# Performance work log

Measured on AMD Instinct MI355X. Metric: run time of the kernel, lower is better.

Reference implementation:

```python
import jax, jax.numpy as jnp
import numpy as np

EMB = 4096
NUM_EXPERTS = 64
TOP_K = 2
TOKENS = 16384


def setup_inputs() -> dict:
    key = jax.random.key(0)
    kx, kw, kb = jax.random.split(key, 3)
    x = jax.random.normal(kx, (TOKENS, EMB), dtype=jnp.float32)
    # nn.Linear(emb_size, num_experts): weight [num_experts, emb], bias [num_experts]
    W = jax.random.normal(kw, (NUM_EXPERTS, EMB), dtype=jnp.float32) / np.sqrt(EMB)
    b = jax.random.normal(kb, (NUM_EXPERTS,), dtype=jnp.float32) * 0.01
    return {"x": x, "W": W, "b": b}


def reference(x, W, b):
    # logits = x @ W.T + b  -> [tokens, num_experts]
    logits = jnp.einsum("td,ed->te", x, W) + b
    topk_val, topk_idx = jax.lax.top_k(logits, TOP_K)  # [tokens, k]
    probs = jax.nn.softmax(topk_val, axis=-1)
    return (topk_idx, probs)
```

## Files before the change

kernel.cpp:

```cpp
#include <hip/hip_runtime.h>

#define TOKENS 16384
#define EMB 4096
#define NEXP 64
#define BK 64

typedef __attribute__((ext_vector_type(8))) short short8;
typedef __attribute__((ext_vector_type(4))) float f32x4;
typedef __attribute__((ext_vector_type(4))) unsigned short ush4;

#define WP_USHORTS (3 * NEXP * EMB)
#define WP_FLOATS  (WP_USHORTS / 2)

__device__ __forceinline__ void gl_lds16(const void* g, void* lds) {
    __builtin_amdgcn_global_load_lds(
        (const __attribute__((address_space(1))) void*)g,
        (__attribute__((address_space(3))) void*)lds, 16, 0, 0);
}

__device__ __forceinline__ void split3(float x, unsigned short& h,
                                       unsigned short& m, unsigned short& l) {
    unsigned u = __float_as_uint(x);
    unsigned r = u + 0x7FFFu + ((u >> 16) & 1u);
    float hF = __uint_as_float(r & 0xFFFF0000u);
    h = (unsigned short)(r >> 16);
    float r1 = x - hF;
    unsigned u1 = __float_as_uint(r1);
    float mF = __uint_as_float(u1 & 0xFFFF0000u);
    m = (unsigned short)(u1 >> 16);
    float r2 = r1 - mF;
    l = (unsigned short)(__float_as_uint(r2) >> 16);
}

__global__ __launch_bounds__(256) void split_w(const float* __restrict__ W,
                                               unsigned short* __restrict__ Wp) {
    const int i = (blockIdx.x * 256 + threadIdx.x) * 4;
    const float4 v = *reinterpret_cast<const float4*>(W + i);
    ush4 h, m, l;
#pragma unroll
    for (int e = 0; e < 4; ++e) {
        unsigned short he, me, le;
        split3(reinterpret_cast<const float*>(&v)[e], he, me, le);
        h[e] = he; m[e] = me; l[e] = le;
    }
    *reinterpret_cast<ush4*>(Wp + i) = h;
    *reinterpret_cast<ush4*>(Wp + NEXP * EMB + i) = m;
    *reinterpret_cast<ush4*>(Wp + 2 * NEXP * EMB + i) = l;
}

template<int S>
__global__ __launch_bounds__(512, 4) void router_mfma(
    const float* __restrict__ x, const unsigned short* __restrict__ Wp,
    float* __restrict__ part)
{
    constexpr int KPER = EMB / S;
    constexpr int NCH  = KPER / BK;

    __shared__ unsigned short sB[3][192][BK];

    const int t  = threadIdx.x;
    const int w  = t >> 6;
    const int l  = t & 63;
    const int lr = l & 15;
    const int lo = l >> 4;
    const int tok0 = blockIdx.x * 128 + w * 16;
    const int kb   = blockIdx.y * KPER;

    const float* ax = x + (size_t)(tok0 + lr) * EMB + kb + lo * 8;

    const unsigned short* gb[3];
#pragma unroll
    for (int p = 0; p < 3; ++p)
        gb[p] = Wp + (size_t)(24 * w + 8 * p + (l >> 3)) * EMB + kb
              + 8 * ((l & 7) ^ ((l >> 3) & 7));

    f32x4 accH[4], accL[4];
#pragma unroll
    for (int et = 0; et < 4; ++et) {
        accH[et] = (f32x4){0.f, 0.f, 0.f, 0.f};
        accL[et] = (f32x4){0.f, 0.f, 0.f, 0.f};
    }

    float4 ac[2][2], an[2][2];
#pragma unroll
    for (int p = 0; p < 3; ++p)
        gl_lds16(gb[p], &sB[0][24 * w + 8 * p][0]);
#pragma unroll
    for (int h = 0; h < 2; ++h) {
        ac[h][0] = *reinterpret_cast<const float4*>(ax + 32 * h);
        ac[h][1] = *reinterpret_cast<const float4*>(ax + 32 * h + 4);
    }
#pragma unroll
    for (int p = 0; p < 3; ++p)
        gl_lds16(gb[p] + BK, &sB[1][24 * w + 8 * p][0]);

    int buf = 0;
#pragma unroll 1
    for (int ks = 0; ks < NCH; ++ks) {
        asm volatile("s_waitcnt vmcnt(3)" ::: "memory");
        __builtin_amdgcn_s_barrier();

        if (ks + 1 < NCH) {
#pragma unroll
            for (int h = 0; h < 2; ++h) {
                an[h][0] = *reinterpret_cast<const float4*>(ax + (ks + 1) * BK + 32 * h);
                an[h][1] = *reinterpret_cast<const float4*>(ax + (ks + 1) * BK + 32 * h + 4);
            }
        }
        if (ks + 2 < NCH) {
            const int sb = (buf == 0) ? 2 : buf - 1;
#pragma unroll
            for (int p = 0; p < 3; ++p)
                gl_lds16(gb[p] + (ks + 2) * BK, &sB[sb][24 * w + 8 * p][0]);
        }
        __builtin_amdgcn_sched_barrier(0);

#pragma unroll
        for (int h = 0; h < 2; ++h) {
            short8 aH, aM, aL;
#pragma unroll
            for (int e = 0; e < 4; ++e) {
                unsigned short he, me, le;
                split3(reinterpret_cast<const float*>(&ac[h][0])[e], he, me, le);
                aH[e] = (short)he; aM[e] = (short)me; aL[e] = (short)le;
                split3(reinterpret_cast<const float*>(&ac[h][1])[e], he, me, le);
                aH[4 + e] = (short)he; aM[4 + e] = (short)me; aL[4 + e] = (short)le;
            }
#pragma unroll
            for (int et = 0; et < 4; ++et) {
                const int sw = (((4 * h + lo) ^ (lr & 7)) * 8);
                const unsigned short* bp = &sB[buf][et * 16 + lr][sw];
                const short8 bH = *reinterpret_cast<const short8*>(bp);
                const short8 bM = *reinterpret_cast<const short8*>(bp + 64 * BK);
                const short8 bL = *reinterpret_cast<const short8*>(bp + 128 * BK);
                accH[et] = __builtin_amdgcn_mfma_f32_16x16x32_bf16(aH, bH, accH[et], 0, 0, 0);
                accL[et] = __builtin_amdgcn_mfma_f32_16x16x32_bf16(aH, bM, accL[et], 0, 0, 0);
                accL[et] = __builtin_amdgcn_mfma_f32_16x16x32_bf16(aM, bH, accL[et], 0, 0, 0);
                accL[et] = __builtin_amdgcn_mfma_f32_16x16x32_bf16(aM, bM, accL[et], 0, 0, 0);
                accL[et] = __builtin_amdgcn_mfma_f32_16x16x32_bf16(aH, bL, accL[et], 0, 0, 0);
                accL[et] = __builtin_amdgcn_mfma_f32_16x16x32_bf16(aL, bH, accL[et], 0, 0, 0);
            }
        }
#pragma unroll
        for (int h = 0; h < 2; ++h) { ac[h][0] = an[h][0]; ac[h][1] = an[h][1]; }
        buf = (buf == 2) ? 0 : buf + 1;
    }

    __syncthreads();
    float* sled = reinterpret_cast<float*>(&sB[0][0][0]) + w * 1024;
#pragma unroll
    for (int et = 0; et < 4; ++et)
#pragma unroll
        for (int j = 0; j < 4; ++j)
            sled[(et * 16 + lr) * 16 + lo * 4 + j] = accH[et][j] + accL[et][j];
#pragma unroll
    for (int r = 0; r < 16; ++r) {
        const int e = 4 * r + lo;
        part[(size_t)(blockIdx.y * NEXP + e) * TOKENS + tok0 + lr]
            = sled[e * 16 + lr];
    }
}

template<int S>
__global__ __launch_bounds__(256) void reduce_topk(
    const float* __restrict__ part, const float* __restrict__ b,
    float* __restrict__ out)
{
    __shared__ double sv[64][4][2];
    __shared__ int    si[64][4][2];
    const int t    = threadIdx.x;
    const int p4   = t & 3;
    const int slot = t >> 2;
    const int tok  = blockIdx.x * 64 + slot;

    double v[16];
#pragma unroll
    for (int j = 0; j < 16; ++j) v[j] = 0.0;
    for (int s = 0; s < S; ++s)
#pragma unroll
        for (int j = 0; j < 16; ++j)
            v[j] += (double)part[(size_t)((s << 6) + (p4 << 4) + j) * TOKENS + tok];
#pragma unroll
    for (int j = 0; j < 16; ++j) v[j] += (double)b[(p4 << 4) + j];

    double v1 = -1e300, v2 = -1e300; int i1 = 0, i2 = 0;
#pragma unroll
    for (int j = 0; j < 16; ++j) {
        const int e = (p4 << 4) + j;
        if (v[j] > v1)      { v2 = v1; i2 = i1; v1 = v[j]; i1 = e; }
        else if (v[j] > v2) { v2 = v[j]; i2 = e; }
    }
    sv[slot][p4][0] = v1; sv[slot][p4][1] = v2;
    si[slot][p4][0] = i1; si[slot][p4][1] = i2;
    __syncthreads();

    if (p4 == 0) {
        double m1 = -1e300, m2 = -1e300; int j1 = 0, j2 = 0;
#pragma unroll
        for (int p = 0; p < 4; ++p)
#pragma unroll
            for (int r = 0; r < 2; ++r) {
                const double vv = sv[slot][p][r]; const int ii = si[slot][p][r];
                if (vv > m1)      { m2 = m1; j2 = j1; m1 = vv; j1 = ii; }
                else if (vv > m2) { m2 = vv; j2 = ii; }
            }
        const float e2  = expf((float)(m2 - m1));
        const float inv = 1.0f / (1.0f + e2);
        out[2 * tok]     = (float)j1;
        out[2 * tok + 1] = (float)j2;
        out[2 * TOKENS + 2 * tok]     = inv;
        out[2 * TOKENS + 2 * tok + 1] = e2 * inv;
    }
}

extern "C" void kernel_launch(void* const* d_in, const int* in_sizes, int n_in,
                              void* d_out, int out_size, void* d_ws, size_t ws_size,
                              hipStream_t stream) {
    const float* x = (const float*)d_in[0];
    const float* W = (const float*)d_in[1];
    const float* b = (const float*)d_in[2];
    float* out = (float*)d_out;
    unsigned short* Wp = (unsigned short*)d_ws;
    float* part = (float*)d_ws + WP_FLOATS;

    split_w<<<dim3(NEXP * EMB / 1024), dim3(256), 0, stream>>>(W, Wp);

    const size_t base = (size_t)WP_FLOATS * 4;
    const size_t per  = (size_t)NEXP * TOKENS * 4;
    if (ws_size >= base + 4 * per) {
        router_mfma<4><<<dim3(TOKENS / 128, 4), dim3(512), 0, stream>>>(x, Wp, part);
        reduce_topk<4><<<dim3(TOKENS / 64), dim3(256), 0, stream>>>(part, b, out);
    } else if (ws_size >= base + 2 * per) {
        router_mfma<2><<<dim3(TOKENS / 128, 2), dim3(512), 0, stream>>>(x, Wp, part);
        reduce_topk<2><<<dim3(TOKENS / 64), dim3(256), 0, stream>>>(part, b, out);
    } else {
        router_mfma<1><<<dim3(TOKENS / 128, 1), dim3(512), 0, stream>>>(x, Wp, part);
        reduce_topk<1><<<dim3(TOKENS / 64), dim3(256), 0, stream>>>(part, b, out);
    }
}
```

Measured before the change: 81.00 us.

## Compute two token tiles per wave to reuse B fragments from LDS

The router GEMM block drops from 8 to 4 waves, and each wave now handles 32 tokens (two 16-row tiles). Each B fragment read from LDS therefore feeds twice as many MFMAs, which halves LDS read traffic per MFMA. The bf16 three-way split is rewritten to pack pairs with v_perm, cutting the ALU work that builds the A fragments. In exchange each thread holds more registers (double the accumulators and A staging), occupancy drops, and the epilogue uses a padded 33-stride LDS transpose.

Result: no change. 81.12 us (+0.2%).

```diff
diff --git a/kernel.cpp b/kernel.cpp
--- a/kernel.cpp
+++ b/kernel.cpp
@@ -32,6 +32,31 @@
     l = (unsigned short)(__float_as_uint(r2) >> 16);
 }
 
+__device__ __forceinline__ void split3_pair(float x0, float x1,
+        unsigned& hw, unsigned& mw, unsigned& lw) {
+    unsigned u0 = __float_as_uint(x0), u1 = __float_as_uint(x1);
+    unsigned r0 = u0 + 0x7FFFu + ((u0 >> 16) & 1u);
+    unsigned r1 = u1 + 0x7FFFu + ((u1 >> 16) & 1u);
+    hw = __builtin_amdgcn_perm(r1, r0, 0x07060302u);
+    float s0 = x0 - __uint_as_float(r0 & 0xFFFF0000u);
+    float s1 = x1 - __uint_as_float(r1 & 0xFFFF0000u);
+    unsigned v0 = __float_as_uint(s0), v1 = __float_as_uint(s1);
+    mw = __builtin_amdgcn_perm(v1, v0, 0x07060302u);
+    float t0 = s0 - __uint_as_float(v0 & 0xFFFF0000u);
+    float t1 = s1 - __uint_as_float(v1 & 0xFFFF0000u);
+    lw = __builtin_amdgcn_perm(__float_as_uint(t1), __float_as_uint(t0), 0x07060302u);
+}
+
+__device__ __forceinline__ void build_frags(const float4& a0, const float4& a1,
+        short8& H, short8& M, short8& L) {
+    union { short8 v; unsigned u[4]; } h_, m_, l_;
+    split3_pair(a0.x, a0.y, h_.u[0], m_.u[0], l_.u[0]);
+    split3_pair(a0.z, a0.w, h_.u[1], m_.u[1], l_.u[1]);
+    split3_pair(a1.x, a1.y, h_.u[2], m_.u[2], l_.u[2]);
+    split3_pair(a1.z, a1.w, h_.u[3], m_.u[3], l_.u[3]);
+    H = h_.v; M = m_.v; L = l_.v;
+}
+
 __global__ __launch_bounds__(256) void split_w(const float* __restrict__ W,
                                                unsigned short* __restrict__ Wp) {
     const int i = (blockIdx.x * 256 + threadIdx.x) * 4;
@@ -49,7 +74,7 @@
 }
 
 template<int S>
-__global__ __launch_bounds__(512, 4) void router_mfma(
+__global__ __launch_bounds__(256, 2) void router_mfma(
     const float* __restrict__ x, const unsigned short* __restrict__ Wp,
     float* __restrict__ part)
 {
@@ -63,101 +88,119 @@
     const int l  = t & 63;
     const int lr = l & 15;
     const int lo = l >> 4;
-    const int tok0 = blockIdx.x * 128 + w * 16;
+    const int tok0 = blockIdx.x * 128 + w * 32;
     const int kb   = blockIdx.y * KPER;
 
-    const float* ax = x + (size_t)(tok0 + lr) * EMB + kb + lo * 8;
-
-    const unsigned short* gb[3];
-#pragma unroll
-    for (int p = 0; p < 3; ++p)
-        gb[p] = Wp + (size_t)(24 * w + 8 * p + (l >> 3)) * EMB + kb
+    const float* ax[2];
+    ax[0] = x + (size_t)(tok0 + lr) * EMB + kb + lo * 8;
+    ax[1] = x + (size_t)(tok0 + 16 + lr) * EMB + kb + lo * 8;
+
+    const unsigned short* gb[6];
+#pragma unroll
+    for (int p = 0; p < 6; ++p)
+        gb[p] = Wp + (size_t)(48 * w + 8 * p + (l >> 3)) * EMB + kb
               + 8 * ((l & 7) ^ ((l >> 3) & 7));
 
-    f32x4 accH[4], accL[4];
-#pragma unroll
-    for (int et = 0; et < 4; ++et) {
-        accH[et] = (f32x4){0.f, 0.f, 0.f, 0.f};
-        accL[et] = (f32x4){0.f, 0.f, 0.f, 0.f};
-    }
-
-    float4 ac[2][2], an[2][2];
-#pragma unroll
-    for (int p = 0; p < 3; ++p)
-        gl_lds16(gb[p], &sB[0][24 * w + 8 * p][0]);
-#pragma unroll
-    for (int h = 0; h < 2; ++h) {
-        ac[h][0] = *reinterpret_cast<const float4*>(ax + 32 * h);
-        ac[h][1] = *reinterpret_cast<const float4*>(ax + 32 * h + 4);
-    }
-#pragma unroll
-    for (int p = 0; p < 3; ++p)
-        gl_lds16(gb[p] + BK, &sB[1][24 * w + 8 * p][0]);
+    f32x4 accH[2][4], accL[2][4];
+#pragma unroll
+    for (int ti = 0; ti < 2; ++ti)
+#pragma unroll
+        for (int et = 0; et < 4; ++et) {
+            accH[ti][et] = (f32x4){0.f, 0.f, 0.f, 0.f};
+            accL[ti][et] = (f32x4){0.f, 0.f, 0.f, 0.f};
+        }
+
+    float4 ac[2][2][2], an[2][2][2];
+#pragma unroll
+    for (int p = 0; p < 6; ++p)
+        gl_lds16(gb[p], &sB[0][48 * w + 8 * p][0]);
+#pragma unroll
+    for (int ti = 0; ti < 2; ++ti)
+#pragma unroll
+        for (int h = 0; h < 2; ++h) {
+            ac[ti][h][0] = *reinterpret_cast<const float4*>(ax[ti] + 32 * h);
+            ac[ti][h][1] = *reinterpret_cast<const float4*>(ax[ti] + 32 * h + 4);
+        }
+#pragma unroll
+    for (int p = 0; p < 6; ++p)
+        gl_lds16(gb[p] + BK, &sB[1][48 * w + 8 * p][0]);
 
     int buf = 0;
 #pragma unroll 1
     for (int ks = 0; ks < NCH; ++ks) {
-        asm volatile("s_waitcnt vmcnt(3)" ::: "memory");
+        asm volatile("s_waitcnt vmcnt(6)" ::: "memory");
         __builtin_amdgcn_s_barrier();
 
         if (ks + 1 < NCH) {
 #pragma unroll
-            for (int h = 0; h < 2; ++h) {
-                an[h][0] = *reinterpret_cast<const float4*>(ax + (ks + 1) * BK + 32 * h);
-                an[h][1] = *reinterpret_cast<const float4*>(ax + (ks + 1) * BK + 32 * h + 4);
-            }
+            for (int ti = 0; ti < 2; ++ti)
+#pragma unroll
+                for (int h = 0; h < 2; ++h) {
+                    an[ti][h][0] = *reinterpret_cast<const float4*>(
+                        ax[ti] + (ks + 1) * BK + 32 * h);
+                    an[ti][h][1] = *reinterpret_cast<const float4*>(
+                        ax[ti] + (ks + 1) * BK + 32 * h + 4);
+                }
         }
         if (ks + 2 < NCH) {
             const int sb = (buf == 0) ? 2 : buf - 1;
 #pragma unroll
-            for (int p = 0; p < 3; ++p)
-                gl_lds16(gb[p] + (ks + 2) * BK, &sB[sb][24 * w + 8 * p][0]);
+            for (int p = 0; p < 6; ++p)
+                gl_lds16(gb[p] + (ks + 2) * BK, &sB[sb][48 * w + 8 * p][0]);
         }
         __builtin_amdgcn_sched_barrier(0);
 
 #pragma unroll
         for (int h = 0; h < 2; ++h) {
-            short8 aH, aM, aL;
-#pragma unroll
-            for (int e = 0; e < 4; ++e) {
-                unsigned short he, me, le;
-                split3(reinterpret_cast<const float*>(&ac[h][0])[e], he, me, le);
-                aH[e] = (short)he; aM[e] = (short)me; aL[e] = (short)le;
-                split3(reinterpret_cast<const float*>(&ac[h][1])[e], he, me, le);
-                aH[4 + e] = (short)he; aM[4 + e] = (short)me; aL[4 + e] = (short)le;
-            }
+            short8 aH0, aM0, aL0, aH1, aM1, aL1;
+            build_frags(ac[0][h][0], ac[0][h][1], aH0, aM0, aL0);
+            build_frags(ac[1][h][0], ac[1][h][1], aH1, aM1, aL1);
+            const int sw = ((4 * h + lo) ^ (lr & 7)) * 8;
 #pragma unroll
             for (int et = 0; et < 4; ++et) {
-                const int sw = (((4 * h + lo) ^ (lr & 7)) * 8);
                 const unsigned short* bp = &sB[buf][et * 16 + lr][sw];
                 const short8 bH = *reinterpret_cast<const short8*>(bp);
                 const short8 bM = *reinterpret_cast<const short8*>(bp + 64 * BK);
                 const short8 bL = *reinterpret_cast<const short8*>(bp + 128 * BK);
-                accH[et] = __builtin_amdgcn_mfma_f32_16x16x32_bf16(aH, bH, accH[et], 0, 0, 0);
-                accL[et] = __builtin_amdgcn_mfma_f32_16x16x32_bf16(aH, bM, accL[et], 0, 0, 0);
-                accL[et] = __builtin_amdgcn_mfma_f32_16x16x32_bf16(aM, bH, accL[et], 0, 0, 0);
-                accL[et] = __builtin_amdgcn_mfma_f32_16x16x32_bf16(aM, bM, accL[et], 0, 0, 0);
-                accL[et] = __builtin_amdgcn_mfma_f32_16x16x32_bf16(aH, bL, accL[et], 0, 0, 0);
-                accL[et] = __builtin_amdgcn_mfma_f32_16x16x32_bf16(aL, bH, accL[et], 0, 0, 0);
+                accH[0][et] = __builtin_amdgcn_mfma_f32_16x16x32_bf16(aH0, bH, accH[0][et], 0, 0, 0);
+                accL[0][et] = __builtin_amdgcn_mfma_f32_16x16x32_bf16(aH0, bM, accL[0][et], 0, 0, 0);
+                accL[0][et] = __builtin_amdgcn_mfma_f32_16x16x32_bf16(aM0, bH, accL[0][et], 0, 0, 0);
+                accL[0][et] = __builtin_amdgcn_mfma_f32_16x16x32_bf16(aM0, bM, accL[0][et], 0, 0, 0);
+                accL[0][et] = __builtin_amdgcn_mfma_f32_16x16x32_bf16(aH0, bL, accL[0][et], 0, 0, 0);
+                accL[0][et] = __builtin_amdgcn_mfma_f32_16x16x32_bf16(aL0, bH, accL[0][et], 0, 0, 0);
+                accH[1][et] = __builtin_amdgcn_mfma_f32_16x16x32_bf16(aH1, bH, accH[1][et], 0, 0, 0);
+                accL[1][et] = __builtin_amdgcn_mfma_f32_16x16x32_bf16(aH1, bM, accL[1][et], 0, 0, 0);
+                accL[1][et] = __builtin_amdgcn_mfma_f32_16x16x32_bf16(aM1, bH, accL[1][et], 0, 0, 0);
+                accL[1][et] = __builtin_amdgcn_mfma_f32_16x16x32_bf16(aM1, bM, accL[1][et], 0, 0, 0);
+                accL[1][et] = __builtin_amdgcn_mfma_f32_16x16x32_bf16(aH1, bL, accL[1][et], 0, 0, 0);
+                accL[1][et] = __builtin_amdgcn_mfma_f32_16x16x32_bf16(aL1, bH, accL[1][et], 0, 0, 0);
             }
         }
 #pragma unroll
-        for (int h = 0; h < 2; ++h) { ac[h][0] = an[h][0]; ac[h][1] = an[h][1]; }
+        for (int ti = 0; ti < 2; ++ti)
+#pragma unroll
+            for (int h = 0; h < 2; ++h) {
+                ac[ti][h][0] = an[ti][h][0];
+                ac[ti][h][1] = an[ti][h][1];
+            }
         buf = (buf == 2) ? 0 : buf + 1;
     }
 
     __syncthreads();
-    float* sled = reinterpret_cast<float*>(&sB[0][0][0]) + w * 1024;
-#pragma unroll
-    for (int et = 0; et < 4; ++et)
-#pragma unroll
-        for (int j = 0; j < 4; ++j)
-            sled[(et * 16 + lr) * 16 + lo * 4 + j] = accH[et][j] + accL[et][j];
-#pragma unroll
-    for (int r = 0; r < 16; ++r) {
-        const int e = 4 * r + lo;
-        part[(size_t)(blockIdx.y * NEXP + e) * TOKENS + tok0 + lr]
-            = sled[e * 16 + lr];
+    float* sled = reinterpret_cast<float*>(&sB[0][0][0]) + w * 2112;
+#pragma unroll
+    for (int ti = 0; ti < 2; ++ti)
+#pragma unroll
+        for (int et = 0; et < 4; ++et)
+#pragma unroll
+            for (int j = 0; j < 4; ++j)
+                sled[(et * 16 + lr) * 33 + ti * 16 + lo * 4 + j]
+                    = accH[ti][et][j] + accL[ti][et][j];
+#pragma unroll
+    for (int r = 0; r < 32; ++r) {
+        const int e = 2 * r + (l >> 5);
+        part[(size_t)(blockIdx.y * NEXP + e) * TOKENS + tok0 + (l & 31)]
+            = sled[e * 33 + (l & 31)];
     }
 }
 
@@ -228,13 +271,13 @@
     const size_t base = (size_t)WP_FLOATS * 4;
     const size_t per  = (size_t)NEXP * TOKENS * 4;
     if (ws_size >= base + 4 * per) {
-        router_mfma<4><<<dim3(TOKENS / 128, 4), dim3(512), 0, stream>>>(x, Wp, part);
+        router_mfma<4><<<dim3(TOKENS / 128, 4), dim3(256), 0, stream>>>(x, Wp, part);
         reduce_topk<4><<<dim3(TOKENS / 64), dim3(256), 0, stream>>>(part, b, out);
     } else if (ws_size >= base + 2 * per) {
-        router_mfma<2><<<dim3(TOKENS / 128, 2), dim3(512), 0, stream>>>(x, Wp, part);
+        router_mfma<2><<<dim3(TOKENS / 128, 2), dim3(256), 0, stream>>>(x, Wp, part);
         reduce_topk<2><<<dim3(TOKENS / 64), dim3(256), 0, stream>>>(part, b, out);
     } else {
-        router_mfma<1><<<dim3(TOKENS / 128, 1), dim3(512), 0, stream>>>(x, Wp, part);
+        router_mfma<1><<<dim3(TOKENS / 128, 1), dim3(256), 0, stream>>>(x, Wp, part);
         reduce_topk<1><<<dim3(TOKENS / 64), dim3(256), 0, stream>>>(part, b, out);
     }
 }
```
